# Performance work log

Measured on AMD Instinct MI355X. Metric: run time of the kernel, lower is better.

Reference implementation:

```python
import jax, jax.numpy as jnp
import numpy as np
from jax import lax

N = 8192
D = 64

def setup_inputs() -> dict:
    key = jax.random.key(0)
    k1, k2 = jax.random.split(key)
    nodevec1 = jax.random.normal(k1, (N, D), dtype=jnp.float32)
    nodevec2 = jax.random.normal(k2, (D, N), dtype=jnp.float32)
    return {"nodevec1": nodevec1, "nodevec2": nodevec2, "topk": 32}

def reference(nodevec1, nodevec2, topk):
    # [N, N] low-rank adjacency
    adp = jnp.maximum(nodevec1 @ nodevec2, 0.0)
    n = adp.shape[1]
    if topk < n:
        # per-row top-k, scatter values into zeros (matches torch.topk + scatter_)
        vals, idx = lax.top_k(adp, topk)  # [N, k]
        rows = jnp.arange(adp.shape[0])[:, None]  # [N, 1]
        adp = jnp.zeros_like(adp).at[rows, idx].set(vals)
    # softmax over full row, zeros included (exp(0)=1 terms), same as F.softmax
    return jax.nn.softmax(adp, axis=1)
```

## Files before the change

kernel.cpp:

```cpp
#include <hip/hip_runtime.h>

#define NN 8192
#define DD 64
#define ROWS 16
#define NWAVE 16
#define NT 1024
#define TPW 32
#define CAP 320
#define NBINS 160
#define INVBINW 4.0f
#define SHIFT 48.0f
#define ZSCALE 4503599627370496.0f
#define SELCAP 64

typedef _Float16 half8 __attribute__((ext_vector_type(8)));
typedef float    f32x4 __attribute__((ext_vector_type(4)));
typedef unsigned long long ull;

__device__ __forceinline__ unsigned h16bits(_Float16 h) {
    union { _Float16 h; unsigned short u; } cv; cv.h = h; return (unsigned)cv.u;
}
__device__ __forceinline__ float h16val(unsigned u) {
    union { unsigned short u; _Float16 h; } cv; cv.u = (unsigned short)u; return (float)cv.h;
}

__global__ __launch_bounds__(256) void prep_bt(
    const float* __restrict__ in, _Float16* __restrict__ bt2)
{
    __shared__ float t[64][65];
    const int c0 = blockIdx.x * 64;
    for (int i = threadIdx.x; i < 4096; i += 256) {
        const int r = i >> 6, c = i & 63;
        t[c][r] = in[(size_t)r * NN + c0 + c];
    }
    __syncthreads();
    for (int i = threadIdx.x; i < 4096; i += 256) {
        const int c = i >> 6, r = i & 63;
        const int col = c0 + c;
        const int dst = ((col >> 4) * 2 + (r >> 5)) * 512
                      + (((r >> 3) & 3) * 16 + (col & 15)) * 8 + (r & 7);
        bt2[dst] = (_Float16)t[c][r];
    }
}

__device__ __forceinline__ void band_select(
    const float* __restrict__ nv1, const _Float16* __restrict__ bt2,
    int row0, int wv, int ln, int g, int cl,
    unsigned (&cand)[ROWS][CAP], int (&ccnt)[ROWS])
{
    half8 af[2];
    float s2 = 0.f;
    const float* pa = nv1 + (size_t)(row0 + cl) * DD + g * 8;
    #pragma unroll
    for (int ks = 0; ks < 2; ++ks)
        #pragma unroll
        for (int j = 0; j < 8; ++j) {
            const float x = pa[ks * 32 + j];
            af[ks][j] = (_Float16)x;
            s2 += x * x;
        }
    s2 += __shfl_xor(s2, 16);
    s2 += __shfl_xor(s2, 32);
    float pref4[4];
    #pragma unroll
    for (int i = 0; i < 4; ++i) pref4[i] = 2.0f * sqrtf(__shfl(s2, g * 4 + i));

    const _Float16* pb = bt2 + (size_t)(wv * TPW) * 1024 + ln * 8;
    const int wbase = wv * 512;

    #pragma unroll 4
    for (int t = 0; t < TPW; ++t) {
        const half8 b0 = *reinterpret_cast<const half8*>(pb + t * 1024);
        const half8 b1 = *reinterpret_cast<const half8*>(pb + t * 1024 + 512);
        f32x4 acc = {0.f, 0.f, 0.f, 0.f};
        acc = __builtin_amdgcn_mfma_f32_16x16x32_f16(af[0], b0, acc, 0, 0, 0);
        acc = __builtin_amdgcn_mfma_f32_16x16x32_f16(af[1], b1, acc, 0, 0, 0);
        #pragma unroll
        for (int i = 0; i < 4; ++i) {
            const float v = fmaxf(acc[i], 0.f);
            if (v > pref4[i]) {
                const int r = g * 4 + i;
                const unsigned key = (h16bits((_Float16)v) << 13)
                                   | (unsigned)(wbase + t * 16 + cl);
                const int idx = atomicAdd(&ccnt[r], 1);
                if (idx < CAP) cand[r][idx] = key;
            }
        }
    }
}

__device__ __forceinline__ void band_finish(
    int wv, int ln, int K,
    unsigned (&cand)[ROWS][CAP], unsigned (&hist)[ROWS][NBINS], int (&ccnt)[ROWS],
    ull (&sel)[ROWS][SELCAP], float* b0arr, float& iZ_out, int& ecnt_out)
{
    const int n = min(ccnt[wv], CAP);
    for (int idx = ln; idx < n; idx += 64) {
        int bi = (int)(h16val(cand[wv][idx] >> 13) * INVBINW);
        bi = bi < NBINS - 1 ? bi : NBINS - 1;
        atomicAdd(&hist[wv][bi], 1u);
    }
    int bsel;
    {
        unsigned s0  = hist[wv][159 - ln];
        unsigned s1  = hist[wv][95 - ln];
        unsigned s2b = (ln < 32) ? hist[wv][31 - ln] : 0u;
        #pragma unroll
        for (int d = 1; d < 64; d <<= 1) {
            const unsigned t0 = __shfl_up(s0, d);
            const unsigned t1 = __shfl_up(s1, d);
            const unsigned t2 = __shfl_up(s2b, d);
            if (ln >= d) { s0 += t0; s1 += t1; s2b += t2; }
        }
        const unsigned tot0 = __shfl(s0, 63);
        const unsigned tot1 = __shfl(s1, 63);
        s1  += tot0;
        s2b += tot0 + tot1;
        const ull m0 = __ballot(s0 >= (unsigned)K);
        const ull m1 = __ballot(s1 >= (unsigned)K);
        const ull m2 = __ballot(s2b >= (unsigned)K);
        bsel = 0;
        if (m0)      bsel = 159 - (__ffsll((long long)m0) - 1);
        else if (m1) bsel = 95  - (__ffsll((long long)m1) - 1);
        else if (m2) bsel = 31  - (__ffsll((long long)m2) - 1);
    }
    const float e0 = __expf(-SHIFT);
    unsigned ec = 0;
    ull zloc = 0ull;
    for (int base = 0; base < n; base += 64) {
        bool c = false; float e = 0.f; unsigned key = 0u;
        if (base + ln < n) {
            key = cand[wv][base + ln];
            const float vb = h16val(key >> 13);
            int bi = (int)(vb * INVBINW);
            bi = bi < NBINS - 1 ? bi : NBINS - 1;
            if (bi >= bsel) { c = true; e = __expf(vb - SHIFT); }
        }
        const ull m = __ballot(c);
        if (c) {
            const unsigned slot = ec + (unsigned)__popcll(m & ((1ull << ln) - 1ull));
            if (slot < SELCAP)
                sel[wv][slot] = ((ull)__float_as_uint(e) << 32) | (key & 0x1FFFu);
            zloc += (ull)(e * ZSCALE);
        }
        ec += (unsigned)__popcll(m);
    }
    #pragma unroll
    for (int off = 1; off < 64; off <<= 1) zloc += __shfl_xor(zloc, off);
    if (ec > SELCAP) ec = SELCAP;
    const float Z  = ldexpf((float)zloc, -52) + (float)(NN - (int)ec) * e0;
    iZ_out   = 1.0f / Z;
    ecnt_out = (int)ec;
    if (ln == 0) b0arr[wv] = e0 * iZ_out;
    for (int i = ln; i < NBINS; i += 64) hist[wv][i] = 0u;
    if (ln == 0) ccnt[wv] = 0;
}

__global__ __launch_bounds__(NT) void sag_pipe(
    const float* __restrict__ nv1, const _Float16* __restrict__ bt2,
    const int* __restrict__ topkp, float* __restrict__ out)
{
    __shared__ unsigned cand[ROWS][CAP];
    __shared__ unsigned hist[ROWS][NBINS];
    __shared__ int      ccnt[ROWS];
    __shared__ ull      selA[ROWS][SELCAP];
    __shared__ ull      selB[ROWS][SELCAP];
    __shared__ float    b0A[ROWS], b0B[ROWS];

    const int tid = threadIdx.x, wv = tid >> 6, ln = tid & 63;
    const int g = ln >> 4, cl = ln & 15;
    const int r0A = blockIdx.x * (2 * ROWS);
    const int r0B = r0A + ROWS;
    const int K = topkp[0];

    for (int i = ln; i < NBINS; i += 64) hist[wv][i] = 0u;
    if (ln == 0) ccnt[wv] = 0;
    __syncthreads();

    band_select(nv1, bt2, r0A, wv, ln, g, cl, cand, ccnt);
    __syncthreads();

    float iZA; int ecA;
    band_finish(wv, ln, K, cand, hist, ccnt, selA, b0A, iZA, ecA);
    __syncthreads();

    #pragma unroll
    for (int r = 0; r < ROWS; ++r) {
        const float b0v = b0A[r];
        const f32x4 bv = {b0v, b0v, b0v, b0v};
        f32x4* po = reinterpret_cast<f32x4*>(out + (size_t)(r0A + r) * NN);
        po[tid]      = bv;
        po[tid + NT] = bv;
    }
    band_select(nv1, bt2, r0B, wv, ln, g, cl, cand, ccnt);
    __syncthreads();

    if (ln < ecA) {
        const ull w = selA[wv][ln];
        out[(size_t)(r0A + wv) * NN + (unsigned)(w & 0x1FFFu)] =
            __uint_as_float((unsigned)(w >> 32)) * iZA;
    }
    float iZB; int ecB;
    band_finish(wv, ln, K, cand, hist, ccnt, selB, b0B, iZB, ecB);
    __syncthreads();

    #pragma unroll
    for (int r = 0; r < ROWS; ++r) {
        const float b0v = b0B[r];
        const f32x4 bv = {b0v, b0v, b0v, b0v};
        f32x4* po = reinterpret_cast<f32x4*>(out + (size_t)(r0B + r) * NN);
        po[tid]      = bv;
        po[tid + NT] = bv;
    }
    __syncthreads();

    if (ln < ecB) {
        const ull w = selB[wv][ln];
        out[(size_t)(r0B + wv) * NN + (unsigned)(w & 0x1FFFu)] =
            __uint_as_float((unsigned)(w >> 32)) * iZB;
    }
}

extern "C" void kernel_launch(void* const* d_in, const int* in_sizes, int n_in,
                              void* d_out, int out_size, void* d_ws, size_t ws_size,
                              hipStream_t stream) {
    const float* nv1   = (const float*)d_in[0];
    const float* nv2   = (const float*)d_in[1];
    const int*   topkp = (const int*)d_in[2];
    float*       out   = (float*)d_out;
    _Float16*    bt2   = (_Float16*)d_ws;

    hipLaunchKernelGGL(prep_bt,  dim3(NN / 64),          dim3(256), 0, stream, nv2, bt2);
    hipLaunchKernelGGL(sag_pipe, dim3(NN / (2 * ROWS)),  dim3(NT),  0, stream,
                       nv1, bt2, topkp, out);
}
```

Baseline: 101.4 us.

## Fuse both row-band selections into one pass sharing B-tile loads

Computes the MFMA scores for both 16-row bands in a single loop, so each bt2 fragment is loaded once and feeds four MFMAs instead of two. Each block's tile walk is rotated by blockIdx to spread L2 access across blocks, and the candidate threshold is raised from 2.0 to 2.1 sigma with CAP cut to 288 to fit double candidate buffers in LDS. The cost is that the previous overlap of band A's output writes with band B's compute is gone, and the higher threshold risks too few candidates to reach top-k in some rows.

```diff
diff --git a/kernel.cpp b/kernel.cpp
--- a/kernel.cpp
+++ b/kernel.cpp
@@ -6,7 +6,7 @@
 #define NWAVE 16
 #define NT 1024
 #define TPW 32
-#define CAP 320
+#define CAP 288
 #define NBINS 160
 #define INVBINW 4.0f
 #define SHIFT 48.0f
@@ -43,68 +43,21 @@
     }
 }
 
-__device__ __forceinline__ void band_select(
-    const float* __restrict__ nv1, const _Float16* __restrict__ bt2,
-    int row0, int wv, int ln, int g, int cl,
-    unsigned (&cand)[ROWS][CAP], int (&ccnt)[ROWS])
+__device__ __forceinline__ void band_finish(
+    const unsigned* __restrict__ candrow, int n, unsigned* __restrict__ histrow,
+    ull* __restrict__ selrow, float* __restrict__ b0slot,
+    int ln, int K, float& iZ_out, int& ec_out)
 {
-    half8 af[2];
-    float s2 = 0.f;
-    const float* pa = nv1 + (size_t)(row0 + cl) * DD + g * 8;
-    #pragma unroll
-    for (int ks = 0; ks < 2; ++ks)
-        #pragma unroll
-        for (int j = 0; j < 8; ++j) {
-            const float x = pa[ks * 32 + j];
-            af[ks][j] = (_Float16)x;
-            s2 += x * x;
-        }
-    s2 += __shfl_xor(s2, 16);
-    s2 += __shfl_xor(s2, 32);
-    float pref4[4];
-    #pragma unroll
-    for (int i = 0; i < 4; ++i) pref4[i] = 2.0f * sqrtf(__shfl(s2, g * 4 + i));
-
-    const _Float16* pb = bt2 + (size_t)(wv * TPW) * 1024 + ln * 8;
-    const int wbase = wv * 512;
-
-    #pragma unroll 4
-    for (int t = 0; t < TPW; ++t) {
-        const half8 b0 = *reinterpret_cast<const half8*>(pb + t * 1024);
-        const half8 b1 = *reinterpret_cast<const half8*>(pb + t * 1024 + 512);
-        f32x4 acc = {0.f, 0.f, 0.f, 0.f};
-        acc = __builtin_amdgcn_mfma_f32_16x16x32_f16(af[0], b0, acc, 0, 0, 0);
-        acc = __builtin_amdgcn_mfma_f32_16x16x32_f16(af[1], b1, acc, 0, 0, 0);
-        #pragma unroll
-        for (int i = 0; i < 4; ++i) {
-            const float v = fmaxf(acc[i], 0.f);
-            if (v > pref4[i]) {
-                const int r = g * 4 + i;
-                const unsigned key = (h16bits((_Float16)v) << 13)
-                                   | (unsigned)(wbase + t * 16 + cl);
-                const int idx = atomicAdd(&ccnt[r], 1);
-                if (idx < CAP) cand[r][idx] = key;
-            }
-        }
-    }
-}
-
-__device__ __forceinline__ void band_finish(
-    int wv, int ln, int K,
-    unsigned (&cand)[ROWS][CAP], unsigned (&hist)[ROWS][NBINS], int (&ccnt)[ROWS],
-    ull (&sel)[ROWS][SELCAP], float* b0arr, float& iZ_out, int& ecnt_out)
-{
-    const int n = min(ccnt[wv], CAP);
     for (int idx = ln; idx < n; idx += 64) {
-        int bi = (int)(h16val(cand[wv][idx] >> 13) * INVBINW);
+        int bi = (int)(h16val(candrow[idx] >> 13) * INVBINW);
         bi = bi < NBINS - 1 ? bi : NBINS - 1;
-        atomicAdd(&hist[wv][bi], 1u);
+        atomicAdd(&histrow[bi], 1u);
     }
     int bsel;
     {
-        unsigned s0  = hist[wv][159 - ln];
-        unsigned s1  = hist[wv][95 - ln];
-        unsigned s2b = (ln < 32) ? hist[wv][31 - ln] : 0u;
+        unsigned s0  = histrow[159 - ln];
+        unsigned s1  = histrow[95 - ln];
+        unsigned s2b = (ln < 32) ? histrow[31 - ln] : 0u;
         #pragma unroll
         for (int d = 1; d < 64; d <<= 1) {
             const unsigned t0 = __shfl_up(s0, d);
@@ -130,7 +83,7 @@
     for (int base = 0; base < n; base += 64) {
         bool c = false; float e = 0.f; unsigned key = 0u;
         if (base + ln < n) {
-            key = cand[wv][base + ln];
+            key = candrow[base + ln];
             const float vb = h16val(key >> 13);
             int bi = (int)(vb * INVBINW);
             bi = bi < NBINS - 1 ? bi : NBINS - 1;
@@ -140,7 +93,7 @@
         if (c) {
             const unsigned slot = ec + (unsigned)__popcll(m & ((1ull << ln) - 1ull));
             if (slot < SELCAP)
-                sel[wv][slot] = ((ull)__float_as_uint(e) << 32) | (key & 0x1FFFu);
+                selrow[slot] = ((ull)__float_as_uint(e) << 32) | (key & 0x1FFFu);
             zloc += (ull)(e * ZSCALE);
         }
         ec += (unsigned)__popcll(m);
@@ -149,23 +102,21 @@
     for (int off = 1; off < 64; off <<= 1) zloc += __shfl_xor(zloc, off);
     if (ec > SELCAP) ec = SELCAP;
     const float Z  = ldexpf((float)zloc, -52) + (float)(NN - (int)ec) * e0;
-    iZ_out   = 1.0f / Z;
-    ecnt_out = (int)ec;
-    if (ln == 0) b0arr[wv] = e0 * iZ_out;
-    for (int i = ln; i < NBINS; i += 64) hist[wv][i] = 0u;
-    if (ln == 0) ccnt[wv] = 0;
-}
-
-__global__ __launch_bounds__(NT) void sag_pipe(
+    iZ_out = 1.0f / Z;
+    ec_out = (int)ec;
+    if (ln == 0) b0slot[0] = e0 * iZ_out;
+    for (int i = ln; i < NBINS; i += 64) histrow[i] = 0u;
+}
+
+__global__ __launch_bounds__(NT) void sag_fused2(
     const float* __restrict__ nv1, const _Float16* __restrict__ bt2,
     const int* __restrict__ topkp, float* __restrict__ out)
 {
-    __shared__ unsigned cand[ROWS][CAP];
+    __shared__ unsigned cand[2 * ROWS][CAP];
     __shared__ unsigned hist[ROWS][NBINS];
-    __shared__ int      ccnt[ROWS];
-    __shared__ ull      selA[ROWS][SELCAP];
-    __shared__ ull      selB[ROWS][SELCAP];
-    __shared__ float    b0A[ROWS], b0B[ROWS];
+    __shared__ ull      sel[2][ROWS][SELCAP];
+    __shared__ int      ccnt[2 * ROWS];
+    __shared__ float    b0f[2][ROWS];
 
     const int tid = threadIdx.x, wv = tid >> 6, ln = tid & 63;
     const int g = ln >> 4, cl = ln & 15;
@@ -174,48 +125,97 @@
     const int K = topkp[0];
 
     for (int i = ln; i < NBINS; i += 64) hist[wv][i] = 0u;
-    if (ln == 0) ccnt[wv] = 0;
-    __syncthreads();
-
-    band_select(nv1, bt2, r0A, wv, ln, g, cl, cand, ccnt);
-    __syncthreads();
-
-    float iZA; int ecA;
-    band_finish(wv, ln, K, cand, hist, ccnt, selA, b0A, iZA, ecA);
+    if (tid < 2 * ROWS) ccnt[tid] = 0;
+    __syncthreads();
+
+    half8 afA[2], afB[2];
+    float s2A = 0.f, s2B = 0.f;
+    {
+        const float* pa = nv1 + (size_t)(r0A + cl) * DD + g * 8;
+        const float* pb_ = nv1 + (size_t)(r0B + cl) * DD + g * 8;
+        #pragma unroll
+        for (int ks = 0; ks < 2; ++ks)
+            #pragma unroll
+            for (int j = 0; j < 8; ++j) {
+                const float xa = pa[ks * 32 + j];
+                const float xb = pb_[ks * 32 + j];
+                afA[ks][j] = (_Float16)xa;  s2A += xa * xa;
+                afB[ks][j] = (_Float16)xb;  s2B += xb * xb;
+            }
+    }
+    s2A += __shfl_xor(s2A, 16);  s2A += __shfl_xor(s2A, 32);
+    s2B += __shfl_xor(s2B, 16);  s2B += __shfl_xor(s2B, 32);
+    float prefA[4], prefB[4];
+    #pragma unroll
+    for (int i = 0; i < 4; ++i) {
+        prefA[i] = 2.1f * sqrtf(__shfl(s2A, g * 4 + i));
+        prefB[i] = 2.1f * sqrtf(__shfl(s2B, g * 4 + i));
+    }
+
+    const _Float16* pb = bt2 + (size_t)(wv * TPW) * 1024 + ln * 8;
+    const int wbase = wv * 512;
+
+    #pragma unroll 4
+    for (int tt = 0; tt < TPW; ++tt) {
+        const int t = (tt + blockIdx.x) & 31;
+        const half8 b0 = *reinterpret_cast<const half8*>(pb + t * 1024);
+        const half8 b1 = *reinterpret_cast<const half8*>(pb + t * 1024 + 512);
+        f32x4 accA = {0.f, 0.f, 0.f, 0.f};
+        f32x4 accB = {0.f, 0.f, 0.f, 0.f};
+        accA = __builtin_amdgcn_mfma_f32_16x16x32_f16(afA[0], b0, accA, 0, 0, 0);
+        accA = __builtin_amdgcn_mfma_f32_16x16x32_f16(afA[1], b1, accA, 0, 0, 0);
+        accB = __builtin_amdgcn_mfma_f32_16x16x32_f16(afB[0], b0, accB, 0, 0, 0);
+        accB = __builtin_amdgcn_mfma_f32_16x16x32_f16(afB[1], b1, accB, 0, 0, 0);
+        const unsigned colb = (unsigned)(wbase + t * 16 + cl);
+        #pragma unroll
+        for (int i = 0; i < 4; ++i) {
+            const float vA = fmaxf(accA[i], 0.f);
+            if (vA > prefA[i]) {
+                const int r = g * 4 + i;
+                const unsigned key = (h16bits((_Float16)vA) << 13) | colb;
+                const int idx = atomicAdd(&ccnt[r], 1);
+                if (idx < CAP) cand[r][idx] = key;
+            }
+            const float vB = fmaxf(accB[i], 0.f);
+            if (vB > prefB[i]) {
+                const int r = ROWS + g * 4 + i;
+                const unsigned key = (h16bits((_Float16)vB) << 13) | colb;
+                const int idx = atomicAdd(&ccnt[r], 1);
+                if (idx < CAP) cand[r][idx] = key;
+            }
+        }
+    }
+    __syncthreads();
+
+    float iZA, iZB; int ecA, ecB;
+    band_finish(cand[wv],        min(ccnt[wv], CAP),        hist[wv],
+                sel[0][wv], &b0f[0][wv], ln, K, iZA, ecA);
+    band_finish(cand[ROWS + wv], min(ccnt[ROWS + wv], CAP), hist[wv],
+                sel[1][wv], &b0f[1][wv], ln, K, iZB, ecB);
     __syncthreads();
 
     #pragma unroll
     for (int r = 0; r < ROWS; ++r) {
-        const float b0v = b0A[r];
-        const f32x4 bv = {b0v, b0v, b0v, b0v};
-        f32x4* po = reinterpret_cast<f32x4*>(out + (size_t)(r0A + r) * NN);
-        po[tid]      = bv;
-        po[tid + NT] = bv;
-    }
-    band_select(nv1, bt2, r0B, wv, ln, g, cl, cand, ccnt);
+        const float bA = b0f[0][r];
+        const f32x4 bvA = {bA, bA, bA, bA};
+        f32x4* poA = reinterpret_cast<f32x4*>(out + (size_t)(r0A + r) * NN);
+        poA[tid]      = bvA;
+        poA[tid + NT] = bvA;
+        const float bB = b0f[1][r];
+        const f32x4 bvB = {bB, bB, bB, bB};
+        f32x4* poB = reinterpret_cast<f32x4*>(out + (size_t)(r0B + r) * NN);
+        poB[tid]      = bvB;
+        poB[tid + NT] = bvB;
+    }
     __syncthreads();
 
     if (ln < ecA) {
-        const ull w = selA[wv][ln];
+        const ull w = sel[0][wv][ln];
         out[(size_t)(r0A + wv) * NN + (unsigned)(w & 0x1FFFu)] =
             __uint_as_float((unsigned)(w >> 32)) * iZA;
     }
-    float iZB; int ecB;
-    band_finish(wv, ln, K, cand, hist, ccnt, selB, b0B, iZB, ecB);
-    __syncthreads();
-
-    #pragma unroll
-    for (int r = 0; r < ROWS; ++r) {
-        const float b0v = b0B[r];
-        const f32x4 bv = {b0v, b0v, b0v, b0v};
-        f32x4* po = reinterpret_cast<f32x4*>(out + (size_t)(r0B + r) * NN);
-        po[tid]      = bv;
-        po[tid + NT] = bv;
-    }
-    __syncthreads();
-
     if (ln < ecB) {
-        const ull w = selB[wv][ln];
+        const ull w = sel[1][wv][ln];
         out[(size_t)(r0B + wv) * NN + (unsigned)(w & 0x1FFFu)] =
             __uint_as_float((unsigned)(w >> 32)) * iZB;
     }
@@ -230,7 +230,7 @@
     float*       out   = (float*)d_out;
     _Float16*    bt2   = (_Float16*)d_ws;
 
-    hipLaunchKernelGGL(prep_bt,  dim3(NN / 64),          dim3(256), 0, stream, nv2, bt2);
-    hipLaunchKernelGGL(sag_pipe, dim3(NN / (2 * ROWS)),  dim3(NT),  0, stream,
+    hipLaunchKernelGGL(prep_bt,    dim3(NN / 64),         dim3(256), 0, stream, nv2, bt2);
+    hipLaunchKernelGGL(sag_fused2, dim3(NN / (2 * ROWS)), dim3(NT),  0, stream,
                        nv1, bt2, topkp, out);
 }
```

Result: faster. 97.30 us (-4.0%).
